# Performance work log

Measured on AMD Instinct MI355X. Metric: run time of the kernel, lower is better.

## Reference

```python
import jax, jax.numpy as jnp
import numpy as np

KH, KW = 3, 3
STRIDE = (1, 1)
PAD = (1, 1)
DIL = (1, 1)
DG = 1  # num_deformable_groups


def _out_size(h, pad, dil, k, stride):
    return (h + 2 * pad - (dil * (k - 1) + 1)) // stride + 1


def setup_inputs() -> dict:
    key = jax.random.key(0)
    k1, k2, k3 = jax.random.split(key, 3)
    B, Cin, H, W = 8, 128, 64, 64
    Cout = 128
    Ho = _out_size(H, PAD[0], DIL[0], KH, STRIDE[0])
    Wo = _out_size(W, PAD[1], DIL[1], KW, STRIDE[1])
    x = jax.random.normal(k1, (B, Cin, H, W), jnp.float32)
    offset = jax.random.normal(k2, (B, 2 * DG * KH * KW, Ho, Wo), jnp.float32)
    n = Cin * KH * KW
    stdv = 1.0 / np.sqrt(n)
    weight = jax.random.uniform(k3, (Cout, Cin, KH, KW), jnp.float32, -stdv, stdv)
    return {"x": x, "offset": offset, "weight": weight}


def deform_conv2d(x, offset, weight):
    B, Cin, H, W = x.shape
    Cout, _, kh, kw = weight.shape
    K = kh * kw
    Ho = _out_size(H, PAD[0], DIL[0], kh, STRIDE[0])
    Wo = _out_size(W, PAD[1], DIL[1], kw, STRIDE[1])
    G = DG
    Cg = Cin // G

    # base sampling grid per kernel tap: [kh,kw,Ho,Wo]
    by = (jnp.arange(kh) * DIL[0])[:, None, None, None] + (jnp.arange(Ho) * STRIDE[0] - PAD[0])[None, None, :, None]
    bx = (jnp.arange(kw) * DIL[1])[None, :, None, None] + (jnp.arange(Wo) * STRIDE[1] - PAD[1])[None, None, None, :]
    by = jnp.broadcast_to(by, (kh, kw, Ho, Wo)).reshape(K, Ho, Wo).astype(x.dtype)
    bx = jnp.broadcast_to(bx, (kh, kw, Ho, Wo)).reshape(K, Ho, Wo).astype(x.dtype)

    # offset layout: channel = g*2*K + 2*k + {0: dy, 1: dx}
    off = offset.reshape(B, G, K, 2, Ho, Wo)
    py = by[None, None] + off[:, :, :, 0]  # [B,G,K,Ho,Wo]
    px = bx[None, None] + off[:, :, :, 1]

    y0 = jnp.floor(py).astype(jnp.int32)
    x0 = jnp.floor(px).astype(jnp.int32)
    wy = (py - y0).reshape(B, G, 1, -1)  # fractional parts, [B,G,1,K*Ho*Wo]
    wx = (px - x0).reshape(B, G, 1, -1)

    xg = x.reshape(B, G, Cg, H * W)
    N = K * Ho * Wo

    def gather(yi, xi):
        valid = ((yi >= 0) & (yi < H) & (xi >= 0) & (xi < W)).reshape(B, G, 1, N)
        idx = (jnp.clip(yi, 0, H - 1) * W + jnp.clip(xi, 0, W - 1)).reshape(B, G, 1, N)
        v = jnp.take_along_axis(xg, jnp.broadcast_to(idx, (B, G, Cg, N)), axis=3)
        return v * valid.astype(x.dtype)

    v00 = gather(y0, x0)
    v01 = gather(y0, x0 + 1)
    v10 = gather(y0 + 1, x0)
    v11 = gather(y0 + 1, x0 + 1)

    cols = (v00 * (1 - wy) * (1 - wx) + v01 * (1 - wy) * wx
            + v10 * wy * (1 - wx) + v11 * wy * wx)
    cols = cols.reshape(B, G, Cg, K, Ho, Wo)  # deformable im2col columns

    wr = weight.reshape(Cout, G, Cg, K)
    return jnp.einsum('ogck,bgcknm->bonm', wr, cols)


def reference(x, offset, weight):
    return deform_conv2d(x, offset, weight)
```

## Files before the change

### kernel.cpp

```cpp
#include <hip/hip_runtime.h>
#include <hip/hip_bf16.h>

typedef __attribute__((ext_vector_type(4))) float f32x4;
typedef __attribute__((ext_vector_type(2))) float f32x2;
typedef __attribute__((ext_vector_type(8))) short s16x8;
typedef __attribute__((ext_vector_type(4))) unsigned int u32x4;

__device__ __forceinline__ unsigned int f2bf(float f) {
  unsigned int u = __float_as_uint(f);
  u += 0x7fffu + ((u >> 16) & 1u);
  return u >> 16;
}
__device__ __forceinline__ f32x2 unpk(unsigned int p) {
  f32x2 r;
  r.x = __uint_as_float(p << 16);
  r.y = __uint_as_float(p & 0xffff0000u);
  return r;
}
__device__ __forceinline__ unsigned int pk_bf16(f32x2 s) {
  __hip_bfloat162 h = __float22bfloat162_rn(make_float2(s.x, s.y));
  unsigned int u;
  __builtin_memcpy(&u, &h, 4);
  return u;
}

__global__ __launch_bounds__(256) void xtrans_kernel(const float* __restrict__ x,
                                                     unsigned short* __restrict__ xt) {
  int t = blockIdx.x * 256 + threadIdx.x;
  int p  = t & 4095;
  int cg = (t >> 12) & 15;
  int b  = t >> 16;
  const float* xp = x + (((size_t)(b * 128 + cg * 8)) << 12) + p;
  unsigned int r[8];
#pragma unroll
  for (int j = 0; j < 8; ++j) r[j] = f2bf(xp[(size_t)j << 12]);
  u32x4 pk;
  pk.x = r[0] | (r[1] << 16);
  pk.y = r[2] | (r[3] << 16);
  pk.z = r[4] | (r[5] << 16);
  pk.w = r[6] | (r[7] << 16);
  *reinterpret_cast<u32x4*>(xt + ((((size_t)b << 12) + p) << 7) + cg * 8) = pk;
}

__global__ __launch_bounds__(256) void wtrans_kernel(const float* __restrict__ w,
                                                     unsigned short* __restrict__ wf) {
  int tid = blockIdx.x * 256 + threadIdx.x;
  int l  = tid & 63;
  int mt = (tid >> 6) & 7;
  int ch = tid >> 9;
  int cc = ch / 9, tap = ch - cc * 9;
  int co = mt * 16 + (l & 15);
  int cb = cc * 32 + (l >> 4) * 8;
  unsigned int r[8];
#pragma unroll
  for (int j = 0; j < 8; ++j)
    r[j] = f2bf(w[(co * 128 + cb + j) * 9 + tap]);
  u32x4 pk;
  pk.x = r[0] | (r[1] << 16);
  pk.y = r[2] | (r[3] << 16);
  pk.z = r[4] | (r[5] << 16);
  pk.w = r[6] | (r[7] << 16);
  *reinterpret_cast<u32x4*>(wf + (size_t)tid * 8) = pk;
}

__global__ __launch_bounds__(512, 1) void deform_kernel(const unsigned short* __restrict__ xt,
                                                        const float* __restrict__ off,
                                                        const unsigned short* __restrict__ wf,
                                                        float* __restrict__ out) {
  __shared__ __align__(16) unsigned char sWin[8 * 17408];
  __shared__ int    sPos[1152];
  __shared__ float4 sWt[1152];

  const int tid = threadIdx.x;
  const int bid = blockIdx.x;
  const int b   = bid & 7;
  const int ho0 = (bid >> 3) * 2;
  const int r0  = min(max(ho0 - 3, 0), 56);

  for (int r = tid; r < 1152; r += 512) {
    int row = (r >= 576) ? 1 : 0;
    int rr  = r - row * 576;
    int tap = rr >> 6, wo = rr & 63;
    int ho = ho0 + row;
    float dy = off[((b * 18 + 2 * tap)     * 64 + ho) * 64 + wo];
    float dx = off[((b * 18 + 2 * tap + 1) * 64 + ho) * 64 + wo];
    float py = (float)(ho + (tap / 3) - 1) + dy;
    float px = (float)(wo + (tap % 3) - 1) + dx;
    float fy = floorf(py), fx = floorf(px);
    int y0 = (int)fy, x0 = (int)fx;
    float wy = py - fy, wx = px - fx;
    float wt = (y0 >= 0 && y0 < 64) ? (1.f - wy) : 0.f;
    float wb = (y0 + 1 >= 0 && y0 + 1 < 64) ? wy : 0.f;
    int y0c = min(max(y0, 0), 63), y1c = min(max(y0 + 1, 0), 63);
    int bx; float wl, wr;
    if (x0 >= 0 && x0 <= 62)      { bx = x0; wl = 1.f - wx; wr = wx;       }
    else if (x0 == -1)            { bx = 0;  wl = wx;       wr = 0.f;      }
    else if (x0 == 63)            { bx = 62; wl = 0.f;      wr = 1.f - wx; }
    else                          { bx = 0;  wl = 0.f;      wr = 0.f;      }
    sPos[r] = (y0c * 64 + bx) | ((y1c != y0c) ? (1 << 15) : 0);
    sWt[r]  = make_float4(wt * wl, wt * wr, wb * wl, wb * wr);
  }

  {
    const unsigned short* xrow = xt + ((size_t)b << 19) + ((size_t)r0 << 13);
#pragma unroll
    for (int it = 0; it < 16; ++it) {
      int idx = it * 512 + tid;
      int c = idx & 15;
      int p = (idx >> 4) & 63;
      int r = idx >> 10;
      u32x4 v;
      __builtin_memcpy(&v, xrow + (((size_t)(r * 64 + p)) << 7) + c * 8, 16);
      *reinterpret_cast<u32x4*>(&sWin[r * 17408 + p * 272 + c * 16]) = v;
    }
  }
  __syncthreads();

  const int l   = tid & 63;
  const int w   = tid >> 6;
  const int ks  = w & 3;
  const int row = w >> 2;
  const int ln  = l & 15;
  const int kg  = l >> 4;
  const int koff = ks * 64 + kg * 16;
  const int ho  = ho0 + row;

  const unsigned short* xtb = xt + ((size_t)b << 19) + ks * 32 + kg * 8;
  const unsigned short* wfb = wf + (size_t)l * 8;

  f32x4 acc[4][8] = {};

  for (int tap = 0; tap < 9; ++tap) {
    const int ch = ks * 9 + tap;

    s16x8 A[8];
    const unsigned short* wp = wfb + (size_t)(ch * 8) * 512;
#pragma unroll
    for (int mt = 0; mt < 8; ++mt)
      A[mt] = *reinterpret_cast<const s16x8*>(wp + (size_t)mt * 512);

#pragma unroll
    for (int pg = 0; pg < 4; ++pg) {
      const int e = row * 576 + tap * 64 + pg * 16 + ln;
      const int    pp = sPos[e];
      const float4 wv = sWt[e];

      const int aX = pp & 4095;
      const int aY = aX + ((pp >> 9) & 64);
      const int tx  = aX & 63;
      const int twr = (aX >> 6) - r0;
      const int bwr = (aY >> 6) - r0;
      const bool tin = (unsigned)twr < 8u;
      const bool bin = (unsigned)bwr < 8u;

      u32x4 T0, T1, B0, B1;
      {
        int laT = (tin ? twr : 0) * 17408 + tx * 272 + koff;
        __builtin_memcpy(&T0, &sWin[laT],       16);
        __builtin_memcpy(&T1, &sWin[laT + 272], 16);
        int laB = (bin ? bwr : 0) * 17408 + tx * 272 + koff;
        __builtin_memcpy(&B0, &sWin[laB],       16);
        __builtin_memcpy(&B1, &sWin[laB + 272], 16);
      }
      if (!tin) {
        const unsigned short* p0 = xtb + ((size_t)aX << 7);
        __builtin_memcpy(&T0, p0,       16);
        __builtin_memcpy(&T1, p0 + 128, 16);
      }
      if (!bin) {
        const unsigned short* p1 = xtb + ((size_t)aY << 7);
        __builtin_memcpy(&B0, p1,       16);
        __builtin_memcpy(&B1, p1 + 128, 16);
      }

      u32x4 pk;
#pragma unroll
      for (int d = 0; d < 4; ++d) {
        f32x2 s = wv.x * unpk(T0[d]) + wv.y * unpk(T1[d])
                + wv.z * unpk(B0[d]) + wv.w * unpk(B1[d]);
        pk[d] = pk_bf16(s);
      }
      s16x8 bfrag;
      __builtin_memcpy(&bfrag, &pk, 16);

#pragma unroll
      for (int mt = 0; mt < 8; ++mt)
        acc[pg][mt] = __builtin_amdgcn_mfma_f32_16x16x32_bf16(A[mt], bfrag,
                                                              acc[pg][mt], 0, 0, 0);
    }
  }

  float* sF = reinterpret_cast<float*>(sWin);
#define WR_LDS                                                                 \
  { _Pragma("unroll") for (int pg = 0; pg < 4; ++pg)                           \
    _Pragma("unroll") for (int mt = 0; mt < 8; ++mt)                           \
      *reinterpret_cast<f32x4*>(&sF[row * 8448 + (pg * 16 + ln) * 132 + mt * 16 + kg * 4]) = acc[pg][mt]; }
#define RD_LDS                                                                 \
  { _Pragma("unroll") for (int pg = 0; pg < 4; ++pg)                           \
    _Pragma("unroll") for (int mt = 0; mt < 8; ++mt) {                         \
      f32x4 v = *reinterpret_cast<const f32x4*>(&sF[row * 8448 + (pg * 16 + ln) * 132 + mt * 16 + kg * 4]); \
      acc[pg][mt] += v; } }

  __syncthreads();
  if (ks == 1) WR_LDS
  __syncthreads();
  if (ks == 0) RD_LDS
  __syncthreads();
  if (ks == 3) WR_LDS
  __syncthreads();
  if (ks == 2) RD_LDS
  __syncthreads();
  if (ks == 2) WR_LDS
  __syncthreads();
  if (ks == 0) RD_LDS
#undef WR_LDS
#undef RD_LDS

  {
    const int b2 = 16896 + row * 8704;
    if (ks == 0) {
#pragma unroll
      for (int pg = 0; pg < 4; ++pg)
#pragma unroll
        for (int mt = 0; mt < 8; ++mt)
#pragma unroll
          for (int rg = 0; rg < 4; ++rg)
            sF[b2 + (mt * 16 + kg * 4 + rg) * 68 + pg * 16 + ln] = acc[pg][mt][rg];
    }
    __syncthreads();
    if (ks == 0) {
      const int q4  = l & 15;
      const int ch2 = l >> 4;
      float* ob = out + (((size_t)b * 128) * 64 + ho) * 64 + q4 * 4;
#pragma unroll
      for (int i = 0; i < 32; ++i) {
        int co = ch2 * 32 + i;
        f32x4 v = *reinterpret_cast<const f32x4*>(&sF[b2 + co * 68 + q4 * 4]);
        *reinterpret_cast<f32x4*>(ob + (size_t)co * 4096) = v;
      }
    }
  }
}

extern "C" void kernel_launch(void* const* d_in, const int* in_sizes, int n_in,
                              void* d_out, int out_size, void* d_ws, size_t ws_size,
                              hipStream_t stream) {
  (void)in_sizes; (void)n_in; (void)out_size; (void)ws_size;
  const float* x   = (const float*)d_in[0];
  const float* off = (const float*)d_in[1];
  const float* w   = (const float*)d_in[2];
  float* out = (float*)d_out;
  unsigned short* xt = (unsigned short*)d_ws;
  unsigned short* wf = (unsigned short*)d_ws + (8388608 / 2);

  xtrans_kernel<<<2048, 256, 0, stream>>>(x, xt);
  wtrans_kernel<<<72, 256, 0, stream>>>(w, wf);
  deform_kernel<<<256, 512, 0, stream>>>(xt, off, wf, out);
}
```

Baseline: 108.0 us.

## Switch to fp16 with packed half2 bilinear interpolation and XOR-swizzled LDS window

Converts the transposed input and weights from bf16 to fp16, so bilinear interpolation runs as packed half2 FMAs in place of unpacking to fp32 and repacking with rounding. Sampling weights are stored as half2 pairs, which halves that LDS table. The LDS window drops its 272-byte padded row stride for a 256-byte stride with a rotating channel-chunk swizzle to avoid bank conflicts. The risks are lower accuracy from accumulating the interpolation in fp16 and fp16 overflow on large inputs.

```diff
diff --git a/kernel.cpp b/kernel.cpp
--- a/kernel.cpp
+++ b/kernel.cpp
@@ -1,24 +1,22 @@
 #include <hip/hip_runtime.h>
-#include <hip/hip_bf16.h>
+#include <hip/hip_fp16.h>
 
 typedef __attribute__((ext_vector_type(4))) float f32x4;
-typedef __attribute__((ext_vector_type(2))) float f32x2;
-typedef __attribute__((ext_vector_type(8))) short s16x8;
+typedef __attribute__((ext_vector_type(8))) _Float16 f16x8;
 typedef __attribute__((ext_vector_type(4))) unsigned int u32x4;
 
-__device__ __forceinline__ unsigned int f2bf(float f) {
-  unsigned int u = __float_as_uint(f);
-  u += 0x7fffu + ((u >> 16) & 1u);
-  return u >> 16;
-}
-__device__ __forceinline__ f32x2 unpk(unsigned int p) {
-  f32x2 r;
-  r.x = __uint_as_float(p << 16);
-  r.y = __uint_as_float(p & 0xffff0000u);
-  return r;
-}
-__device__ __forceinline__ unsigned int pk_bf16(f32x2 s) {
-  __hip_bfloat162 h = __float22bfloat162_rn(make_float2(s.x, s.y));
+__device__ __forceinline__ unsigned short f2h(float f) {
+  __half h = __float2half_rn(f);
+  unsigned short u;
+  __builtin_memcpy(&u, &h, 2);
+  return u;
+}
+__device__ __forceinline__ __half2 h2_of(unsigned int u) {
+  __half2 h;
+  __builtin_memcpy(&h, &u, 4);
+  return h;
+}
+__device__ __forceinline__ unsigned int u_of(__half2 h) {
   unsigned int u;
   __builtin_memcpy(&u, &h, 4);
   return u;
@@ -33,7 +31,7 @@
   const float* xp = x + (((size_t)(b * 128 + cg * 8)) << 12) + p;
   unsigned int r[8];
 #pragma unroll
-  for (int j = 0; j < 8; ++j) r[j] = f2bf(xp[(size_t)j << 12]);
+  for (int j = 0; j < 8; ++j) r[j] = f2h(xp[(size_t)j << 12]);
   u32x4 pk;
   pk.x = r[0] | (r[1] << 16);
   pk.y = r[2] | (r[3] << 16);
@@ -54,7 +52,7 @@
   unsigned int r[8];
 #pragma unroll
   for (int j = 0; j < 8; ++j)
-    r[j] = f2bf(w[(co * 128 + cb + j) * 9 + tap]);
+    r[j] = f2h(w[(co * 128 + cb + j) * 9 + tap]);
   u32x4 pk;
   pk.x = r[0] | (r[1] << 16);
   pk.y = r[2] | (r[3] << 16);
@@ -67,9 +65,9 @@
                                                         const float* __restrict__ off,
                                                         const unsigned short* __restrict__ wf,
                                                         float* __restrict__ out) {
-  __shared__ __align__(16) unsigned char sWin[8 * 17408];
-  __shared__ int    sPos[1152];
-  __shared__ float4 sWt[1152];
+  __shared__ __align__(16) unsigned char sWin[137216];
+  __shared__ int   sPos[1152];
+  __shared__ uint2 sWt[1152];
 
   const int tid = threadIdx.x;
   const int bid = blockIdx.x;
@@ -98,7 +96,12 @@
     else if (x0 == 63)            { bx = 62; wl = 0.f;      wr = 1.f - wx; }
     else                          { bx = 0;  wl = 0.f;      wr = 0.f;      }
     sPos[r] = (y0c * 64 + bx) | ((y1c != y0c) ? (1 << 15) : 0);
-    sWt[r]  = make_float4(wt * wl, wt * wr, wb * wl, wb * wr);
+    __half2 tp = __floats2half2_rn(wt * wl, wt * wr);
+    __half2 bp = __floats2half2_rn(wb * wl, wb * wr);
+    uint2 ww;
+    ww.x = u_of(tp);
+    ww.y = u_of(bp);
+    sWt[r] = ww;
   }
 
   {
@@ -111,7 +114,7 @@
       int r = idx >> 10;
       u32x4 v;
       __builtin_memcpy(&v, xrow + (((size_t)(r * 64 + p)) << 7) + c * 8, 16);
-      *reinterpret_cast<u32x4*>(&sWin[r * 17408 + p * 272 + c * 16]) = v;
+      *reinterpret_cast<u32x4*>(&sWin[r * 16384 + p * 256 + (((c + p) & 15) << 4)]) = v;
     }
   }
   __syncthreads();
@@ -122,7 +125,7 @@
   const int row = w >> 2;
   const int ln  = l & 15;
   const int kg  = l >> 4;
-  const int koff = ks * 64 + kg * 16;
+  const int c16 = ks * 4 + kg;
   const int ho  = ho0 + row;
 
   const unsigned short* xtb = xt + ((size_t)b << 19) + ks * 32 + kg * 8;
@@ -133,17 +136,17 @@
   for (int tap = 0; tap < 9; ++tap) {
     const int ch = ks * 9 + tap;
 
-    s16x8 A[8];
+    f16x8 A[8];
     const unsigned short* wp = wfb + (size_t)(ch * 8) * 512;
 #pragma unroll
     for (int mt = 0; mt < 8; ++mt)
-      A[mt] = *reinterpret_cast<const s16x8*>(wp + (size_t)mt * 512);
+      A[mt] = *reinterpret_cast<const f16x8*>(wp + (size_t)mt * 512);
 
 #pragma unroll
     for (int pg = 0; pg < 4; ++pg) {
       const int e = row * 576 + tap * 64 + pg * 16 + ln;
-      const int    pp = sPos[e];
-      const float4 wv = sWt[e];
+      const int   pp = sPos[e];
+      const uint2 ww = sWt[e];
 
       const int aX = pp & 4095;
       const int aY = aX + ((pp >> 9) & 64);
@@ -155,12 +158,13 @@
 
       u32x4 T0, T1, B0, B1;
       {
-        int laT = (tin ? twr : 0) * 17408 + tx * 272 + koff;
-        __builtin_memcpy(&T0, &sWin[laT],       16);
-        __builtin_memcpy(&T1, &sWin[laT + 272], 16);
-        int laB = (bin ? bwr : 0) * 17408 + tx * 272 + koff;
-        __builtin_memcpy(&B0, &sWin[laB],       16);
-        __builtin_memcpy(&B1, &sWin[laB + 272], 16);
+        int cT0 = ((c16 + tx) & 15) << 4, cT1 = ((c16 + tx + 1) & 15) << 4;
+        int baseT = (tin ? twr : 0) * 16384 + tx * 256;
+        __builtin_memcpy(&T0, &sWin[baseT + cT0],       16);
+        __builtin_memcpy(&T1, &sWin[baseT + 256 + cT1], 16);
+        int baseB = (bin ? bwr : 0) * 16384 + tx * 256;
+        __builtin_memcpy(&B0, &sWin[baseB + cT0],       16);
+        __builtin_memcpy(&B1, &sWin[baseB + 256 + cT1], 16);
       }
       if (!tin) {
         const unsigned short* p0 = xtb + ((size_t)aX << 7);
@@ -173,20 +177,26 @@
         __builtin_memcpy(&B1, p1 + 128, 16);
       }
 
+      const __half2 wtl = __half2half2(__low2half(h2_of(ww.x)));
+      const __half2 wtr = __half2half2(__high2half(h2_of(ww.x)));
+      const __half2 wbl = __half2half2(__low2half(h2_of(ww.y)));
+      const __half2 wbr = __half2half2(__high2half(h2_of(ww.y)));
       u32x4 pk;
 #pragma unroll
       for (int d = 0; d < 4; ++d) {
-        f32x2 s = wv.x * unpk(T0[d]) + wv.y * unpk(T1[d])
-                + wv.z * unpk(B0[d]) + wv.w * unpk(B1[d]);
-        pk[d] = pk_bf16(s);
-      }
-      s16x8 bfrag;
+        __half2 s = __hmul2(wtl, h2_of(T0[d]));
+        s = __hfma2(wtr, h2_of(T1[d]), s);
+        s = __hfma2(wbl, h2_of(B0[d]), s);
+        s = __hfma2(wbr, h2_of(B1[d]), s);
+        pk[d] = u_of(s);
+      }
+      f16x8 bfrag;
       __builtin_memcpy(&bfrag, &pk, 16);
 
 #pragma unroll
       for (int mt = 0; mt < 8; ++mt)
-        acc[pg][mt] = __builtin_amdgcn_mfma_f32_16x16x32_bf16(A[mt], bfrag,
-                                                              acc[pg][mt], 0, 0, 0);
+        acc[pg][mt] = __builtin_amdgcn_mfma_f32_16x16x32_f16(A[mt], bfrag,
+                                                             acc[pg][mt], 0, 0, 0);
     }
   }
 
```

Result: faster. 102.5 us (-5.1%).
